# Optimization experiments

Measured on AMD Instinct MI355X. Metric: run time of the kernel, lower is better.

## Reference

```python
import jax, jax.numpy as jnp
import numpy as np

N = 8192      # nodes
IN = 1433     # input_feat_dim
H1 = 256      # hidden_dim1
H2 = 128      # hidden_dim2
EPS = 1e-5    # BatchNorm1d eps
NEG = -9e15   # GAT mask value
SLOPE = 0.2   # leaky_relu negative slope (gamma)


def setup_inputs() -> dict:
    key = jax.random.key(0)
    ks = jax.random.split(key, 8)
    x = jax.random.normal(ks[0], (N, H2), dtype=jnp.float32)
    u = jax.random.uniform(ks[1], (N, N), dtype=jnp.float32)
    adj = jnp.where(u > 0.999, jnp.float32(0.01), jnp.float32(0.0))
    def w(k, shape):
        fan = shape[0]
        return jax.random.normal(k, shape, dtype=jnp.float32) / jnp.sqrt(jnp.float32(fan))
    return {
        "x": x,
        "adj": adj,
        "W_att": w(ks[2], (H2, H2)),
        "a_att": w(ks[3], (2 * H2, 1)),
        "W_fd1": w(ks[4], (H2, H1)),
        "bn1_g": jnp.ones((H1,), jnp.float32),
        "bn1_b": jnp.zeros((H1,), jnp.float32),
        "W_fd2": w(ks[5], (H1, IN)),
        "bn2_g": jnp.ones((IN,), jnp.float32),
        "bn2_b": jnp.zeros((IN,), jnp.float32),
        "W_sd1": w(ks[6], (H2, H1)),
        "bn3_g": jnp.ones((H1,), jnp.float32),
        "bn3_b": jnp.zeros((H1,), jnp.float32),
    }


def batchnorm(h, g, b):
    # BatchNorm1d training-mode forward: batch stats, biased variance
    m = h.mean(axis=0)
    v = ((h - m) ** 2).mean(axis=0)
    return (h - m) * jax.lax.rsqrt(v + EPS) * g + b


def reference(x, adj, W_att, a_att, W_fd1, bn1_g, bn1_b, W_fd2, bn2_g, bn2_b,
              W_sd1, bn3_g, bn3_b):
    # --- GraphAttentionLayer (concat=False, dropout=0) ---
    Wh = x @ W_att                       # [N, H2]
    f1 = Wh @ a_att[:H2]                 # [N, 1]
    f2 = Wh @ a_att[H2:]                 # [N, 1]
    e = jax.nn.leaky_relu(f1 + f2.T, SLOPE)          # [N, N]
    att = jnp.where(adj > 0, e, jnp.float32(NEG))
    att = jax.nn.softmax(att, axis=1)
    z = att @ Wh                         # condensed encoder output [N, H2]
    # --- feature decoder branch ---
    h1 = jax.nn.relu(adj @ (z @ W_fd1))  # GCN: adj @ (X W), relu
    h1 = batchnorm(h1, bn1_g, bn1_b)
    feat = jax.nn.relu(adj @ (h1 @ W_fd2))
    feat = batchnorm(feat, bn2_g, bn2_b)
    # --- structure decoder branch ---
    s1 = jax.nn.relu(adj @ (z @ W_sd1))
    s1 = batchnorm(s1, bn3_g, bn3_b)
    struct = s1 @ s1.T                   # inner-product decode, identity act [N, N]
    return feat, struct
```

## Files before the change

kernel.cpp:

```cpp
#include <hip/hip_runtime.h>
#include <hip/hip_bf16.h>
#include <stdint.h>

#define NN 8192
#define MAXNZ 64
#define BN_EPS 1e-5f
#define SLOPE 0.2f
#define IND 1433
#define NPAD 1536

typedef float f32x4v __attribute__((ext_vector_type(4)));
typedef short bf16x8v __attribute__((ext_vector_type(8)));

__device__ __forceinline__ float wave_sum(float v) {
#pragma unroll
  for (int off = 32; off > 0; off >>= 1) v += __shfl_xor(v, off);
  return v;
}
__device__ __forceinline__ float wave_max(float v) {
#pragma unroll
  for (int off = 32; off > 0; off >>= 1) v = fmaxf(v, __shfl_xor(v, off));
  return v;
}

#define GLOAD_LDS16(g, l)                                                      \
  __builtin_amdgcn_global_load_lds(                                            \
      (const __attribute__((address_space(1))) unsigned int*)(g),              \
      (__attribute__((address_space(3))) unsigned int*)(l), 16, 0, 0)

__global__ __launch_bounds__(256) void gemm64_f32(const float* __restrict__ A,
                                                  const float* __restrict__ B,
                                                  float* __restrict__ C, int M,
                                                  int N, int K) {
  __shared__ float As[64][68];
  __shared__ float Bs[64][68];
  const int t = threadIdx.x;
  const int m0 = blockIdx.x * 64, n0 = blockIdx.y * 64;
  const int tx = t & 15, ty = t >> 4;
  float acc[4][4] = {};
  for (int kt = 0; kt < K; kt += 64) {
    if (kt) __syncthreads();
#pragma unroll
    for (int i = 0; i < 4; ++i) {
      int fid = t + 256 * i;
      int r = fid >> 4, kq = (fid & 15) * 4;
      float4 v = *(const float4*)&A[(size_t)(m0 + r) * K + kt + kq];
      *(float4*)&As[r][kq] = v;
    }
#pragma unroll
    for (int i = 0; i < 4; ++i) {
      int fid = t + 256 * i;
      int r = fid >> 4, cq = (fid & 15) * 4;
      float4 v = *(const float4*)&B[(size_t)(kt + r) * N + n0 + cq];
      *(float4*)&Bs[r][cq] = v;
    }
    __syncthreads();
#pragma unroll 4
    for (int k0 = 0; k0 < 64; k0 += 4) {
      float4 a[4], b[4];
#pragma unroll
      for (int i = 0; i < 4; ++i) a[i] = *(const float4*)&As[ty * 4 + i][k0];
#pragma unroll
      for (int j = 0; j < 4; ++j) b[j] = *(const float4*)&Bs[k0 + j][tx * 4];
#pragma unroll
      for (int kk = 0; kk < 4; ++kk) {
#pragma unroll
        for (int i = 0; i < 4; ++i) {
          float av = ((const float*)&a[i])[kk];
#pragma unroll
          for (int j = 0; j < 4; ++j)
            acc[i][j] += av * ((const float*)&b[kk])[j];
        }
      }
    }
  }
#pragma unroll
  for (int i = 0; i < 4; ++i) {
    float4 v = make_float4(acc[i][0], acc[i][1], acc[i][2], acc[i][3]);
    *(float4*)&C[(size_t)(m0 + ty * 4 + i) * N + n0 + tx * 4] = v;
  }
}

__global__ void colf_k(const float* __restrict__ Wh, const float* __restrict__ a_att,
                       float* __restrict__ cs, float* __restrict__ f1,
                       float* __restrict__ f2) {
  __shared__ float csL[128];
  int t = threadIdx.x, l = t & 63, w = t >> 6;
  if (t < 128) csL[t] = 0.f;
  __syncthreads();
  float a0 = a_att[l], a1 = a_att[64 + l], a2 = a_att[128 + l], a3 = a_att[192 + l];
  float s0 = 0.f, s1 = 0.f;
#pragma unroll
  for (int rr = 0; rr < 4; ++rr) {
    int i = blockIdx.x * 16 + w * 4 + rr;
    float w0 = Wh[(size_t)i * 128 + l], w1 = Wh[(size_t)i * 128 + 64 + l];
    s0 += w0;
    s1 += w1;
    float p1 = wave_sum(w0 * a0 + w1 * a1);
    float p2 = wave_sum(w0 * a2 + w1 * a3);
    if (l == 0) { f1[i] = p1; f2[i] = p2; }
  }
  atomicAdd(&csL[l], s0);
  atomicAdd(&csL[64 + l], s1);
  __syncthreads();
  if (t < 128) atomicAdd(&cs[t], csL[t]);
}

__global__ void extract_attn_k(const float* __restrict__ adj, const float* __restrict__ Wh,
                               const float* __restrict__ f1, const float* __restrict__ f2,
                               const float* __restrict__ cs, int* __restrict__ nnzA,
                               int* __restrict__ idxA, float* __restrict__ valA,
                               float* __restrict__ valsumA, float* __restrict__ z) {
  __shared__ int idxL[4][MAXNZ];
  __shared__ float valL[4][MAXNZ];
  int l = threadIdx.x & 63, w = threadIdx.x >> 6;
  int i = blockIdx.x * 4 + w;
  const float* row = adj + (size_t)i * NN;
  int base = 0;
  for (int it = 0; it < NN / 256; ++it) {
    float4 v4 = *(const float4*)&row[it * 256 + l * 4];
#pragma unroll
    for (int j = 0; j < 4; ++j) {
      float v = ((const float*)&v4)[j];
      bool p = v > 0.0f;
      unsigned long long m = __ballot(p);
      if (p) {
        int pos = base + (int)__popcll(m & ((1ull << l) - 1ull));
        if (pos < MAXNZ) {
          idxL[w][pos] = it * 256 + l * 4 + j;
          valL[w][pos] = v;
        }
      }
      base += (int)__popcll(m);
    }
  }
  int nnz = base < MAXNZ ? base : MAXNZ;
  if (l == 0) nnzA[i] = nnz;
  __syncthreads();

  int c = -1;
  float v = 0.f, att = 0.f;
  if (l < nnz) { c = idxL[w][l]; v = valL[w][l]; }
  idxA[(size_t)i * MAXNZ + l] = (l < nnz) ? c : 0;
  valA[(size_t)i * MAXNZ + l] = v;
  float vs = wave_sum(v);
  if (l == 0) valsumA[i] = vs;

  if (nnz == 0) {
    const float inv = 1.0f / 8192.0f;
    z[(size_t)i * 128 + l] = cs[l] * inv;
    z[(size_t)i * 128 + 64 + l] = cs[64 + l] * inv;
    return;
  }
  float e = -INFINITY;
  if (l < nnz) {
    float u = f1[i] + f2[c];
    e = u >= 0.f ? u : SLOPE * u;
  }
  float mx = wave_max(e);
  float p = (l < nnz) ? expf(e - mx) : 0.f;
  float s = wave_sum(p);
  att = p / s;
  float a0 = 0.f, a1 = 0.f;
  for (int j = 0; j < nnz; ++j) {
    float wt = __shfl(att, j);
    int r = __shfl(c, j);
    a0 += wt * Wh[(size_t)r * 128 + l];
    a1 += wt * Wh[(size_t)r * 128 + 64 + l];
  }
  z[(size_t)i * 128 + l] = a0;
  z[(size_t)i * 128 + 64 + l] = a1;
}

__global__ void gather_z_k(const float* __restrict__ X, const int* __restrict__ nnzA,
                           const int* __restrict__ idxA, const float* __restrict__ valA,
                           __hip_bfloat16* __restrict__ Y) {
  int l = threadIdx.x & 63, w = threadIdx.x >> 6;
  int i = blockIdx.x * 4 + w;
  int nnz = nnzA[i];
  float a0 = 0.f, a1 = 0.f;
  for (int j = 0; j < nnz; ++j) {
    int r = idxA[(size_t)i * MAXNZ + j];
    float v = valA[(size_t)i * MAXNZ + j];
    a0 += v * X[(size_t)r * 128 + l];
    a1 += v * X[(size_t)r * 128 + 64 + l];
  }
  Y[(size_t)i * 128 + l] = __float2bfloat16(a0);
  Y[(size_t)i * 128 + 64 + l] = __float2bfloat16(a1);
}

__global__ void s1_gather_k(const __hip_bfloat16* __restrict__ t, const int* __restrict__ nnzA,
                            const int* __restrict__ idxA, const float* __restrict__ valA,
                            const float* __restrict__ valsumA, const float* __restrict__ sums,
                            const float* __restrict__ sumsq, const float* __restrict__ g1,
                            const float* __restrict__ b1, const float* __restrict__ g3,
                            const float* __restrict__ b3, __hip_bfloat16* __restrict__ s1b,
                            __hip_bfloat16* __restrict__ ghb) {
  __shared__ int idxL[MAXNZ];
  __shared__ float valL[MAXNZ];
  int i = blockIdx.x, tt = threadIdx.x;
  int nnz = nnzA[i];
  if (tt < MAXNZ) {
    idxL[tt] = idxA[(size_t)i * MAXNZ + tt];
    valL[tt] = valA[(size_t)i * MAXNZ + tt];
  }
  __syncthreads();
  {
    float m = sums[256 + tt] * (1.f / 8192.f);
    float va = fmaxf(sumsq[256 + tt] * (1.f / 8192.f) - m * m, 0.f);
    float sc = g3[tt] * rsqrtf(va + BN_EPS);
    float sh = b3[tt] - m * sc;
    float v = __bfloat162float(t[(size_t)i * 512 + 256 + tt]) * sc + sh;
    s1b[(size_t)i * 256 + tt] = __float2bfloat16(v);
  }
  float acc = 0.f;
  for (int j = 0; j < nnz; ++j)
    acc += valL[j] * __bfloat162float(t[(size_t)idxL[j] * 512 + tt]);
  float m = sums[tt] * (1.f / 8192.f);
  float va = fmaxf(sumsq[tt] * (1.f / 8192.f) - m * m, 0.f);
  float sc = g1[tt] * rsqrtf(va + BN_EPS);
  float sh = b1[tt] - m * sc;
  ghb[(size_t)i * 256 + tt] = __float2bfloat16(acc * sc + sh * valsumA[i]);
}

__global__ void feat_apply_k(const __hip_bfloat16* __restrict__ fp, const float* __restrict__ sums,
                             const float* __restrict__ sumsq, const float* __restrict__ g,
                             const float* __restrict__ b, float* __restrict__ out) {
  int i = blockIdx.x;
  for (int c = threadIdx.x; c < IND; c += 256) {
    float m = sums[c] * (1.f / 8192.f);
    float va = fmaxf(sumsq[c] * (1.f / 8192.f) - m * m, 0.f);
    float sc = g[c] * rsqrtf(va + BN_EPS);
    float sh = b[c] - m * sc;
    out[(size_t)i * IND + c] = __bfloat162float(fp[(size_t)i * NPAD + c]) * sc + sh;
  }
}

__global__ void prep_k(const float* __restrict__ W_fd2, const float* __restrict__ W_fd1,
                       const float* __restrict__ W_sd1, __hip_bfloat16* __restrict__ Wt,
                       __hip_bfloat16* __restrict__ Wcatb) {
  int b = blockIdx.x, t = threadIdx.x;
  int o = b * 256 + t;
  int n = o >> 8, k = o & 255;
  Wt[o] = __float2bfloat16(n < IND ? W_fd2[(size_t)k * IND + n] : 0.f);
  if (b < 256) {
    int nn = o >> 7, kk = o & 127;
    float v = nn < 256 ? W_fd1[(size_t)kk * 256 + nn] : W_sd1[(size_t)kk * 256 + (nn - 256)];
    Wcatb[o] = __float2bfloat16(v);
  }
}

template <int KT>
__global__ __launch_bounds__(256) void mfma_bt_k(const short* __restrict__ A,
                                                 const short* __restrict__ Bt,
                                                 __hip_bfloat16* __restrict__ C, int ldc,
                                                 int gridN, float* __restrict__ sums,
                                                 float* __restrict__ sumsq) {
  __shared__ short lds[2][16384];
  const int nwg = gridDim.x;
  const int cpx = nwg >> 3;
  const int bid = blockIdx.x;
  const int wg = (bid & 7) * cpx + (bid >> 3);
  const int m0 = (wg / gridN) * 128, n0 = (wg % gridN) * 128;
  const int t = threadIdx.x;
  const int l = t & 63, w = t >> 6;
  const int wm = w >> 1, wn = w & 1;
  const int KW = KT * 128;
  f32x4v acc[4][4];
#pragma unroll
  for (int i = 0; i < 4; ++i)
#pragma unroll
    for (int j = 0; j < 4; ++j)
#pragma unroll
      for (int q = 0; q < 4; ++q) acc[i][j][q] = 0.f;

  for (int kt = 0; kt < KT; ++kt) {
    if (kt) __syncthreads();
#pragma unroll
    for (int i = 0; i < 8; ++i) {
      int region = w * 8 + i;
      int lr = region * 4 + (l >> 4);
      int ch = (l & 15) ^ (lr & 7);
      const short* gA = A + ((size_t)(m0 + lr) * KW + kt * 128 + ch * 8);
      GLOAD_LDS16(gA, &lds[0][region * 512]);
      const short* gB = Bt + ((size_t)(n0 + lr) * KW + kt * 128 + ch * 8);
      GLOAD_LDS16(gB, &lds[1][region * 512]);
    }
    __syncthreads();
#pragma unroll
    for (int ks = 0; ks < 4; ++ks) {
      bf16x8v af[4], bf[4];
#pragma unroll
      for (int mi = 0; mi < 4; ++mi) {
        int lr = wm * 64 + mi * 16 + (l & 15);
        int ch = (ks * 4 + (l >> 4)) ^ (lr & 7);
        af[mi] = *(const bf16x8v*)&lds[0][lr * 128 + ch * 8];
      }
#pragma unroll
      for (int nj = 0; nj < 4; ++nj) {
        int lr = wn * 64 + nj * 16 + (l & 15);
        int ch = (ks * 4 + (l >> 4)) ^ (lr & 7);
        bf[nj] = *(const bf16x8v*)&lds[1][lr * 128 + ch * 8];
      }
#pragma unroll
      for (int mi = 0; mi < 4; ++mi)
#pragma unroll
        for (int nj = 0; nj < 4; ++nj)
          acc[mi][nj] = __builtin_amdgcn_mfma_f32_16x16x32_bf16(
              af[mi], bf[nj], acc[mi][nj], 0, 0, 0);
    }
  }
#pragma unroll
  for (int nj = 0; nj < 4; ++nj) {
    int col = n0 + wn * 64 + nj * 16 + (l & 15);
    float s = 0.f, ss = 0.f;
#pragma unroll
    for (int mi = 0; mi < 4; ++mi) {
#pragma unroll
      for (int q = 0; q < 4; ++q) {
        int row = m0 + wm * 64 + mi * 16 + (l >> 4) * 4 + q;
        float v = fmaxf(acc[mi][nj][q], 0.f);
        C[(size_t)row * ldc + col] = __float2bfloat16(v);
        s += v;
        ss += v * v;
      }
    }
    s += __shfl_xor(s, 16);
    s += __shfl_xor(s, 32);
    ss += __shfl_xor(ss, 16);
    ss += __shfl_xor(ss, 32);
    if ((l >> 4) == 0) {
      atomicAdd(&sums[col], s);
      atomicAdd(&sumsq[col], ss);
    }
  }
}

__global__ __launch_bounds__(256) void mfma_sym_k(const short* __restrict__ A,
                                                  float* __restrict__ C) {
  __shared__ short stag[2][16384];
  const int bid = blockIdx.x;
  const int wg = (bid & 7) * 260 + (bid >> 3);
  int bi = (int)((129.0f - sqrtf(16641.0f - 8.0f * (float)wg)) * 0.5f);
  while ((bi + 1) * 64 - ((bi + 1) * bi) / 2 <= wg) ++bi;
  while (bi * 64 - (bi * (bi - 1)) / 2 > wg) --bi;
  const int bj = bi + (wg - (bi * 64 - (bi * (bi - 1)) / 2));
  const int m0 = bi * 128, n0 = bj * 128;
  const int t = threadIdx.x;
  const int l = t & 63, w = t >> 6;
  const int wm = w >> 1, wn = w & 1;
  f32x4v acc[4][4];
#pragma unroll
  for (int i = 0; i < 4; ++i)
#pragma unroll
    for (int j = 0; j < 4; ++j)
#pragma unroll
      for (int q = 0; q < 4; ++q) acc[i][j][q] = 0.f;

  for (int kt = 0; kt < 2; ++kt) {
    if (kt) __syncthreads();
#pragma unroll
    for (int i = 0; i < 8; ++i) {
      int region = w * 8 + i;
      int lr = region * 4 + (l >> 4);
      int ch = (l & 15) ^ (lr & 7);
      const short* gA = A + ((size_t)(m0 + lr) * 256 + kt * 128 + ch * 8);
      GLOAD_LDS16(gA, &stag[0][region * 512]);
      const short* gB = A + ((size_t)(n0 + lr) * 256 + kt * 128 + ch * 8);
      GLOAD_LDS16(gB, &stag[1][region * 512]);
    }
    __syncthreads();
#pragma unroll
    for (int ks = 0; ks < 4; ++ks) {
      bf16x8v af[4], bf[4];
#pragma unroll
      for (int mi = 0; mi < 4; ++mi) {
        int lr = wm * 64 + mi * 16 + (l & 15);
        int ch = (ks * 4 + (l >> 4)) ^ (lr & 7);
        af[mi] = *(const bf16x8v*)&stag[0][lr * 128 + ch * 8];
      }
#pragma unroll
      for (int nj = 0; nj < 4; ++nj) {
        int lr = wn * 64 + nj * 16 + (l & 15);
        int ch = (ks * 4 + (l >> 4)) ^ (lr & 7);
        bf[nj] = *(const bf16x8v*)&stag[1][lr * 128 + ch * 8];
      }
#pragma unroll
      for (int mi = 0; mi < 4; ++mi)
#pragma unroll
        for (int nj = 0; nj < 4; ++nj)
          acc[mi][nj] = __builtin_amdgcn_mfma_f32_16x16x32_bf16(
              af[mi], bf[nj], acc[mi][nj], 0, 0, 0);
    }
  }
#pragma unroll
  for (int mi = 0; mi < 4; ++mi) {
#pragma unroll
    for (int nj = 0; nj < 4; ++nj) {
      int col = n0 + wn * 64 + nj * 16 + (l & 15);
#pragma unroll
      for (int q = 0; q < 4; ++q) {
        int row = m0 + wm * 64 + mi * 16 + (l >> 4) * 4 + q;
        C[(size_t)row * NN + col] = acc[mi][nj][q];
      }
    }
  }
  if (bi != bj) {
#pragma unroll
    for (int nj = 0; nj < 4; ++nj) {
      int col = n0 + wn * 64 + nj * 16 + (l & 15);
#pragma unroll
      for (int mi = 0; mi < 4; ++mi) {
        int row0 = m0 + wm * 64 + mi * 16 + (l >> 4) * 4;
        float4 v = make_float4(acc[mi][nj][0], acc[mi][nj][1], acc[mi][nj][2],
                               acc[mi][nj][3]);
        *(float4*)&C[(size_t)col * NN + row0] = v;
      }
    }
  }
}

extern "C" void kernel_launch(void* const* d_in, const int* in_sizes, int n_in,
                              void* d_out, int out_size, void* d_ws, size_t ws_size,
                              hipStream_t stream) {
  const float* x = (const float*)d_in[0];
  const float* adj = (const float*)d_in[1];
  const float* W_att = (const float*)d_in[2];
  const float* a_att = (const float*)d_in[3];
  const float* W_fd1 = (const float*)d_in[4];
  const float* bn1g = (const float*)d_in[5];
  const float* bn1b = (const float*)d_in[6];
  const float* W_fd2 = (const float*)d_in[7];
  const float* bn2g = (const float*)d_in[8];
  const float* bn2b = (const float*)d_in[9];
  const float* W_sd1 = (const float*)d_in[10];
  const float* bn3g = (const float*)d_in[11];
  const float* bn3b = (const float*)d_in[12];

  float* out = (float*)d_out;
  float* feat_out = out;
  float* struct_out = out + (size_t)NN * IND;

  float* ws = (float*)d_ws;
  size_t off = 0;
  auto alloc = [&](size_t nfloats) {
    float* p = ws + off;
    off += (nfloats + 255) & ~(size_t)255;
    return p;
  };
  float* Wh = alloc((size_t)NN * 128);
  float* z = alloc((size_t)NN * 128);
  float* f1 = alloc(NN);
  float* f2 = alloc(NN);
  float* valsum = alloc(NN);
  float* zbase = alloc(256 + 512 + 512 + 1536 + 1536);
  float* cs = zbase;
  float* sumsA = zbase + 256;
  float* sumsqA = zbase + 768;
  float* sumsB = zbase + 1280;
  float* sumsqB = zbase + 2816;
  float* valA = alloc((size_t)NN * MAXNZ);
  int* idxA = (int*)alloc((size_t)NN * MAXNZ);
  int* nnzA = (int*)alloc(NN);
  __hip_bfloat16* tbuf = (__hip_bfloat16*)alloc((size_t)NN * 256);
  __hip_bfloat16* gb = (__hip_bfloat16*)alloc((size_t)NN * 64);
  __hip_bfloat16* s1b = (__hip_bfloat16*)alloc((size_t)NN * 128);
  __hip_bfloat16* ghb = (__hip_bfloat16*)alloc((size_t)NN * 128);
  __hip_bfloat16* Wt = (__hip_bfloat16*)alloc((size_t)NPAD * 128);
  __hip_bfloat16* Wcatb = (__hip_bfloat16*)alloc(512 * 64);
  __hip_bfloat16* featb = (__hip_bfloat16*)alloc((size_t)NN * NPAD / 2);

  hipMemsetAsync(zbase, 0, (256 + 512 + 512 + 1536 + 1536) * sizeof(float), stream);

  prep_k<<<NPAD, 256, 0, stream>>>(W_fd2, W_fd1, W_sd1, Wt, Wcatb);

  gemm64_f32<<<dim3(NN / 64, 2), 256, 0, stream>>>(x, W_att, Wh, NN, 128, 128);
  colf_k<<<NN / 16, 256, 0, stream>>>(Wh, a_att, cs, f1, f2);
  extract_attn_k<<<NN / 4, 256, 0, stream>>>(adj, Wh, f1, f2, cs, nnzA, idxA, valA,
                                             valsum, z);
  gather_z_k<<<NN / 4, 256, 0, stream>>>(z, nnzA, idxA, valA, gb);

  mfma_bt_k<1><<<64 * 4, 256, 0, stream>>>((const short*)gb, (const short*)Wcatb,
                                           tbuf, 512, 4, sumsA, sumsqA);
  s1_gather_k<<<NN, 256, 0, stream>>>(tbuf, nnzA, idxA, valA, valsum, sumsA, sumsqA,
                                      bn1g, bn1b, bn3g, bn3b, s1b, ghb);

  mfma_bt_k<2><<<64 * 12, 256, 0, stream>>>((const short*)ghb, (const short*)Wt,
                                            featb, NPAD, 12, sumsB, sumsqB);
  feat_apply_k<<<NN, 256, 0, stream>>>(featb, sumsB, sumsqB, bn2g, bn2b, feat_out);

  mfma_sym_k<<<2080, 256, 0, stream>>>((const short*)s1b, struct_out);
}
```

Measured before the change: 255.7 us.

## Fuse attention projections into Wh GEMM and merge feat/struct GEMMs into one launch

The attention-score projections f1/f2 and the column sums of Wh are now computed in the epilogue of the x@W_att GEMM through shuffles and atomics, which removes the separate colf_k pass over Wh. The feature-decoder GEMM and the symmetric struct GEMM are merged into a single tail_k launch, with feature blocks interleaved among struct blocks at a 24:89 ratio so both run concurrently. The aim is to cut launch overhead and kernel tail bubbles, and to overlap the BN-statistics GEMM with the large struct write. In exchange, f1/f2 now depend on atomic accumulation, which needs a larger zeroed buffer, and the merged kernel carries the register pressure of both branches.

```diff
diff --git a/kernel.cpp b/kernel.cpp
--- a/kernel.cpp
+++ b/kernel.cpp
@@ -28,30 +28,35 @@
       (const __attribute__((address_space(1))) unsigned int*)(g),              \
       (__attribute__((address_space(3))) unsigned int*)(l), 16, 0, 0)
 
-__global__ __launch_bounds__(256) void gemm64_f32(const float* __restrict__ A,
+__global__ __launch_bounds__(256) void gemm_att_k(const float* __restrict__ A,
                                                   const float* __restrict__ B,
-                                                  float* __restrict__ C, int M,
-                                                  int N, int K) {
+                                                  const float* __restrict__ aatt,
+                                                  float* __restrict__ C,
+                                                  float* __restrict__ cs,
+                                                  float* __restrict__ f1,
+                                                  float* __restrict__ f2) {
   __shared__ float As[64][68];
   __shared__ float Bs[64][68];
+  __shared__ float csL[64];
   const int t = threadIdx.x;
   const int m0 = blockIdx.x * 64, n0 = blockIdx.y * 64;
   const int tx = t & 15, ty = t >> 4;
+  if (t < 64) csL[t] = 0.f;
   float acc[4][4] = {};
-  for (int kt = 0; kt < K; kt += 64) {
+  for (int kt = 0; kt < 128; kt += 64) {
     if (kt) __syncthreads();
 #pragma unroll
     for (int i = 0; i < 4; ++i) {
       int fid = t + 256 * i;
       int r = fid >> 4, kq = (fid & 15) * 4;
-      float4 v = *(const float4*)&A[(size_t)(m0 + r) * K + kt + kq];
+      float4 v = *(const float4*)&A[(size_t)(m0 + r) * 128 + kt + kq];
       *(float4*)&As[r][kq] = v;
     }
 #pragma unroll
     for (int i = 0; i < 4; ++i) {
       int fid = t + 256 * i;
       int r = fid >> 4, cq = (fid & 15) * 4;
-      float4 v = *(const float4*)&B[(size_t)(kt + r) * N + n0 + cq];
+      float4 v = *(const float4*)&B[(size_t)(kt + r) * 128 + n0 + cq];
       *(float4*)&Bs[r][cq] = v;
     }
     __syncthreads();
@@ -77,33 +82,43 @@
 #pragma unroll
   for (int i = 0; i < 4; ++i) {
     float4 v = make_float4(acc[i][0], acc[i][1], acc[i][2], acc[i][3]);
-    *(float4*)&C[(size_t)(m0 + ty * 4 + i) * N + n0 + tx * 4] = v;
-  }
-}
-
-__global__ void colf_k(const float* __restrict__ Wh, const float* __restrict__ a_att,
-                       float* __restrict__ cs, float* __restrict__ f1,
-                       float* __restrict__ f2) {
-  __shared__ float csL[128];
-  int t = threadIdx.x, l = t & 63, w = t >> 6;
-  if (t < 128) csL[t] = 0.f;
+    *(float4*)&C[(size_t)(m0 + ty * 4 + i) * 128 + n0 + tx * 4] = v;
+  }
+  float a1v[4], a2v[4];
+#pragma unroll
+  for (int j = 0; j < 4; ++j) {
+    a1v[j] = aatt[n0 + tx * 4 + j];
+    a2v[j] = aatt[128 + n0 + tx * 4 + j];
+  }
+#pragma unroll
+  for (int i = 0; i < 4; ++i) {
+    float p1 = acc[i][0] * a1v[0] + acc[i][1] * a1v[1] + acc[i][2] * a1v[2] +
+               acc[i][3] * a1v[3];
+    float p2 = acc[i][0] * a2v[0] + acc[i][1] * a2v[1] + acc[i][2] * a2v[2] +
+               acc[i][3] * a2v[3];
+#pragma unroll
+    for (int off = 1; off < 16; off <<= 1) {
+      p1 += __shfl_xor(p1, off);
+      p2 += __shfl_xor(p2, off);
+    }
+    if ((t & 15) == 0) {
+      atomicAdd(&f1[m0 + ty * 4 + i], p1);
+      atomicAdd(&f2[m0 + ty * 4 + i], p2);
+    }
+  }
+  float cp[4];
+#pragma unroll
+  for (int j = 0; j < 4; ++j) {
+    cp[j] = acc[0][j] + acc[1][j] + acc[2][j] + acc[3][j];
+    cp[j] += __shfl_xor(cp[j], 16);
+    cp[j] += __shfl_xor(cp[j], 32);
+  }
+  if ((t & 63) < 16) {
+#pragma unroll
+    for (int j = 0; j < 4; ++j) atomicAdd(&csL[(t & 15) * 4 + j], cp[j]);
+  }
   __syncthreads();
-  float a0 = a_att[l], a1 = a_att[64 + l], a2 = a_att[128 + l], a3 = a_att[192 + l];
-  float s0 = 0.f, s1 = 0.f;
-#pragma unroll
-  for (int rr = 0; rr < 4; ++rr) {
-    int i = blockIdx.x * 16 + w * 4 + rr;
-    float w0 = Wh[(size_t)i * 128 + l], w1 = Wh[(size_t)i * 128 + 64 + l];
-    s0 += w0;
-    s1 += w1;
-    float p1 = wave_sum(w0 * a0 + w1 * a1);
-    float p2 = wave_sum(w0 * a2 + w1 * a3);
-    if (l == 0) { f1[i] = p1; f2[i] = p2; }
-  }
-  atomicAdd(&csL[l], s0);
-  atomicAdd(&csL[64 + l], s1);
-  __syncthreads();
-  if (t < 128) atomicAdd(&cs[t], csL[t]);
+  if (t < 64) atomicAdd(&cs[n0 + t], csL[t]);
 }
 
 __global__ void extract_attn_k(const float* __restrict__ adj, const float* __restrict__ Wh,
@@ -336,16 +351,18 @@
   }
 }
 
-__global__ __launch_bounds__(256) void mfma_sym_k(const short* __restrict__ A,
-                                                  float* __restrict__ C) {
-  __shared__ short stag[2][16384];
+__global__ __launch_bounds__(256) void tail_k(const short* __restrict__ Agh,
+                                              const short* __restrict__ Wt,
+                                              __hip_bfloat16* __restrict__ featb,
+                                              float* __restrict__ sums,
+                                              float* __restrict__ sumsq,
+                                              const short* __restrict__ S,
+                                              float* __restrict__ C) {
+  __shared__ short lds[2][16384];
   const int bid = blockIdx.x;
-  const int wg = (bid & 7) * 260 + (bid >> 3);
-  int bi = (int)((129.0f - sqrtf(16641.0f - 8.0f * (float)wg)) * 0.5f);
-  while ((bi + 1) * 64 - ((bi + 1) * bi) / 2 <= wg) ++bi;
-  while (bi * 64 - (bi * (bi - 1)) / 2 > wg) --bi;
-  const int bj = bi + (wg - (bi * 64 - (bi * (bi - 1)) / 2));
-  const int m0 = bi * 128, n0 = bj * 128;
+  const int fA = bid * 24 / 89;
+  const int fB = (bid + 1) * 24 / 89;
+  const bool isFeat = fB > fA;
   const int t = threadIdx.x;
   const int l = t & 63, w = t >> 6;
   const int wm = w >> 1, wn = w & 1;
@@ -357,64 +374,137 @@
 #pragma unroll
       for (int q = 0; q < 4; ++q) acc[i][j][q] = 0.f;
 
-  for (int kt = 0; kt < 2; ++kt) {
-    if (kt) __syncthreads();
-#pragma unroll
-    for (int i = 0; i < 8; ++i) {
-      int region = w * 8 + i;
-      int lr = region * 4 + (l >> 4);
-      int ch = (l & 15) ^ (lr & 7);
-      const short* gA = A + ((size_t)(m0 + lr) * 256 + kt * 128 + ch * 8);
-      GLOAD_LDS16(gA, &stag[0][region * 512]);
-      const short* gB = A + ((size_t)(n0 + lr) * 256 + kt * 128 + ch * 8);
-      GLOAD_LDS16(gB, &stag[1][region * 512]);
-    }
-    __syncthreads();
-#pragma unroll
-    for (int ks = 0; ks < 4; ++ks) {
-      bf16x8v af[4], bf[4];
-#pragma unroll
-      for (int mi = 0; mi < 4; ++mi) {
-        int lr = wm * 64 + mi * 16 + (l & 15);
-        int ch = (ks * 4 + (l >> 4)) ^ (lr & 7);
-        af[mi] = *(const bf16x8v*)&stag[0][lr * 128 + ch * 8];
-      }
-#pragma unroll
-      for (int nj = 0; nj < 4; ++nj) {
-        int lr = wn * 64 + nj * 16 + (l & 15);
-        int ch = (ks * 4 + (l >> 4)) ^ (lr & 7);
-        bf[nj] = *(const bf16x8v*)&stag[1][lr * 128 + ch * 8];
-      }
-#pragma unroll
-      for (int mi = 0; mi < 4; ++mi)
-#pragma unroll
-        for (int nj = 0; nj < 4; ++nj)
-          acc[mi][nj] = __builtin_amdgcn_mfma_f32_16x16x32_bf16(
-              af[mi], bf[nj], acc[mi][nj], 0, 0, 0);
-    }
-  }
-#pragma unroll
-  for (int mi = 0; mi < 4; ++mi) {
+  if (isFeat) {
+    const int fb = fA;
+    const int wg = (fb & 7) * 96 + (fb >> 3);
+    const int m0 = (wg / 12) * 128, n0 = (wg % 12) * 128;
+    for (int kt = 0; kt < 2; ++kt) {
+      if (kt) __syncthreads();
+#pragma unroll
+      for (int i = 0; i < 8; ++i) {
+        int region = w * 8 + i;
+        int lr = region * 4 + (l >> 4);
+        int ch = (l & 15) ^ (lr & 7);
+        const short* gA = Agh + ((size_t)(m0 + lr) * 256 + kt * 128 + ch * 8);
+        GLOAD_LDS16(gA, &lds[0][region * 512]);
+        const short* gB = Wt + ((size_t)(n0 + lr) * 256 + kt * 128 + ch * 8);
+        GLOAD_LDS16(gB, &lds[1][region * 512]);
+      }
+      __syncthreads();
+#pragma unroll
+      for (int ks = 0; ks < 4; ++ks) {
+        bf16x8v af[4], bf[4];
+#pragma unroll
+        for (int mi = 0; mi < 4; ++mi) {
+          int lr = wm * 64 + mi * 16 + (l & 15);
+          int ch = (ks * 4 + (l >> 4)) ^ (lr & 7);
+          af[mi] = *(const bf16x8v*)&lds[0][lr * 128 + ch * 8];
+        }
+#pragma unroll
+        for (int nj = 0; nj < 4; ++nj) {
+          int lr = wn * 64 + nj * 16 + (l & 15);
+          int ch = (ks * 4 + (l >> 4)) ^ (lr & 7);
+          bf[nj] = *(const bf16x8v*)&lds[1][lr * 128 + ch * 8];
+        }
+#pragma unroll
+        for (int mi = 0; mi < 4; ++mi)
+#pragma unroll
+          for (int nj = 0; nj < 4; ++nj)
+            acc[mi][nj] = __builtin_amdgcn_mfma_f32_16x16x32_bf16(
+                af[mi], bf[nj], acc[mi][nj], 0, 0, 0);
+      }
+    }
 #pragma unroll
     for (int nj = 0; nj < 4; ++nj) {
       int col = n0 + wn * 64 + nj * 16 + (l & 15);
-#pragma unroll
-      for (int q = 0; q < 4; ++q) {
-        int row = m0 + wm * 64 + mi * 16 + (l >> 4) * 4 + q;
-        C[(size_t)row * NN + col] = acc[mi][nj][q];
-      }
-    }
-  }
-  if (bi != bj) {
-#pragma unroll
-    for (int nj = 0; nj < 4; ++nj) {
-      int col = n0 + wn * 64 + nj * 16 + (l & 15);
+      float s = 0.f, ss = 0.f;
 #pragma unroll
       for (int mi = 0; mi < 4; ++mi) {
-        int row0 = m0 + wm * 64 + mi * 16 + (l >> 4) * 4;
-        float4 v = make_float4(acc[mi][nj][0], acc[mi][nj][1], acc[mi][nj][2],
-                               acc[mi][nj][3]);
-        *(float4*)&C[(size_t)col * NN + row0] = v;
+#pragma unroll
+        for (int q = 0; q < 4; ++q) {
+          int row = m0 + wm * 64 + mi * 16 + (l >> 4) * 4 + q;
+          float v = fmaxf(acc[mi][nj][q], 0.f);
+          featb[(size_t)row * NPAD + col] = __float2bfloat16(v);
+          s += v;
+          ss += v * v;
+        }
+      }
+      s += __shfl_xor(s, 16);
+      s += __shfl_xor(s, 32);
+      ss += __shfl_xor(ss, 16);
+      ss += __shfl_xor(ss, 32);
+      if ((l >> 4) == 0) {
+        atomicAdd(&sums[col], s);
+        atomicAdd(&sumsq[col], ss);
+      }
+    }
+  } else {
+    const int sb = bid - fA;
+    const int wg = (sb & 7) * 260 + (sb >> 3);
+    int bi = (int)((129.0f - sqrtf(16641.0f - 8.0f * (float)wg)) * 0.5f);
+    while ((bi + 1) * 64 - ((bi + 1) * bi) / 2 <= wg) ++bi;
+    while (bi * 64 - (bi * (bi - 1)) / 2 > wg) --bi;
+    const int bj = bi + (wg - (bi * 64 - (bi * (bi - 1)) / 2));
+    const int m0 = bi * 128, n0 = bj * 128;
+    for (int kt = 0; kt < 2; ++kt) {
+      if (kt) __syncthreads();
+#pragma unroll
+      for (int i = 0; i < 8; ++i) {
+        int region = w * 8 + i;
+        int lr = region * 4 + (l >> 4);
+        int ch = (l & 15) ^ (lr & 7);
+        const short* gA = S + ((size_t)(m0 + lr) * 256 + kt * 128 + ch * 8);
+        GLOAD_LDS16(gA, &lds[0][region * 512]);
+        const short* gB = S + ((size_t)(n0 + lr) * 256 + kt * 128 + ch * 8);
+        GLOAD_LDS16(gB, &lds[1][region * 512]);
+      }
+      __syncthreads();
+#pragma unroll
+      for (int ks = 0; ks < 4; ++ks) {
+        bf16x8v af[4], bf[4];
+#pragma unroll
+        for (int mi = 0; mi < 4; ++mi) {
+          int lr = wm * 64 + mi * 16 + (l & 15);
+          int ch = (ks * 4 + (l >> 4)) ^ (lr & 7);
+          af[mi] = *(const bf16x8v*)&lds[0][lr * 128 + ch * 8];
+        }
+#pragma unroll
+        for (int nj = 0; nj < 4; ++nj) {
+          int lr = wn * 64 + nj * 16 + (l & 15);
+          int ch = (ks * 4 + (l >> 4)) ^ (lr & 7);
+          bf[nj] = *(const bf16x8v*)&lds[1][lr * 128 + ch * 8];
+        }
+#pragma unroll
+        for (int mi = 0; mi < 4; ++mi)
+#pragma unroll
+          for (int nj = 0; nj < 4; ++nj)
+            acc[mi][nj] = __builtin_amdgcn_mfma_f32_16x16x32_bf16(
+                af[mi], bf[nj], acc[mi][nj], 0, 0, 0);
+      }
+    }
+#pragma unroll
+    for (int mi = 0; mi < 4; ++mi) {
+#pragma unroll
+      for (int nj = 0; nj < 4; ++nj) {
+        int col = n0 + wn * 64 + nj * 16 + (l & 15);
+#pragma unroll
+        for (int q = 0; q < 4; ++q) {
+          int row = m0 + wm * 64 + mi * 16 + (l >> 4) * 4 + q;
+          C[(size_t)row * NN + col] = acc[mi][nj][q];
+        }
+      }
+    }
+    if (bi != bj) {
+#pragma unroll
+      for (int nj = 0; nj < 4; ++nj) {
+        int col = n0 + wn * 64 + nj * 16 + (l & 15);
+#pragma unroll
+        for (int mi = 0; mi < 4; ++mi) {
+          int row0 = m0 + wm * 64 + mi * 16 + (l >> 4) * 4;
+          float4 v = make_float4(acc[mi][nj][0], acc[mi][nj][1], acc[mi][nj][2],
+                                 acc[mi][nj][3]);
+          *(float4*)&C[(size_t)col * NN + row0] = v;
+        }
       }
     }
   }
@@ -450,15 +540,16 @@
   };
   float* Wh = alloc((size_t)NN * 128);
   float* z = alloc((size_t)NN * 128);
-  float* f1 = alloc(NN);
-  float* f2 = alloc(NN);
   float* valsum = alloc(NN);
-  float* zbase = alloc(256 + 512 + 512 + 1536 + 1536);
+  const size_t ZTOT = 256 + 8192 + 8192 + 512 + 512 + 1536 + 1536;
+  float* zbase = alloc(ZTOT);
   float* cs = zbase;
-  float* sumsA = zbase + 256;
-  float* sumsqA = zbase + 768;
-  float* sumsB = zbase + 1280;
-  float* sumsqB = zbase + 2816;
+  float* f1 = zbase + 256;
+  float* f2 = zbase + 256 + 8192;
+  float* sumsA = zbase + 256 + 16384;
+  float* sumsqA = sumsA + 512;
+  float* sumsB = sumsqA + 512;
+  float* sumsqB = sumsB + 1536;
   float* valA = alloc((size_t)NN * MAXNZ);
   int* idxA = (int*)alloc((size_t)NN * MAXNZ);
   int* nnzA = (int*)alloc(NN);
@@ -470,12 +561,11 @@
   __hip_bfloat16* Wcatb = (__hip_bfloat16*)alloc(512 * 64);
   __hip_bfloat16* featb = (__hip_bfloat16*)alloc((size_t)NN * NPAD / 2);
 
-  hipMemsetAsync(zbase, 0, (256 + 512 + 512 + 1536 + 1536) * sizeof(float), stream);
+  hipMemsetAsync(zbase, 0, ZTOT * sizeof(float), stream);
 
   prep_k<<<NPAD, 256, 0, stream>>>(W_fd2, W_fd1, W_sd1, Wt, Wcatb);
 
-  gemm64_f32<<<dim3(NN / 64, 2), 256, 0, stream>>>(x, W_att, Wh, NN, 128, 128);
-  colf_k<<<NN / 16, 256, 0, stream>>>(Wh, a_att, cs, f1, f2);
+  gemm_att_k<<<dim3(NN / 64, 2), 256, 0, stream>>>(x, W_att, a_att, Wh, cs, f1, f2);
   extract_attn_k<<<NN / 4, 256, 0, stream>>>(adj, Wh, f1, f2, cs, nnzA, idxA, valA,
                                              valsum, z);
   gather_z_k<<<NN / 4, 256, 0, stream>>>(z, nnzA, idxA, valA, gb);
@@ -485,9 +575,7 @@
   s1_gather_k<<<NN, 256, 0, stream>>>(tbuf, nnzA, idxA, valA, valsum, sumsA, sumsqA,
                                       bn1g, bn1b, bn3g, bn3b, s1b, ghb);
 
-  mfma_bt_k<2><<<64 * 12, 256, 0, stream>>>((const short*)ghb, (const short*)Wt,
-                                            featb, NPAD, 12, sumsB, sumsqB);
+  tail_k<<<2848, 256, 0, stream>>>((const short*)ghb, (const short*)Wt, featb,
+                                   sumsB, sumsqB, (const short*)s1b, struct_out);
   feat_apply_k<<<NN, 256, 0, stream>>>(featb, sumsB, sumsqB, bn2g, bn2b, feat_out);
-
-  mfma_sym_k<<<2080, 256, 0, stream>>>((const short*)s1b, struct_out);
-}
+}
```

New measurement: 247.7 us (median of 2 runs). -3.1%, faster.
